# Kernel tuning notes

Measured on AMD Instinct MI355X. Metric: run time of the kernel, lower is better.

The kernel has to match this reference:

```python
import jax, jax.numpy as jnp
import numpy as np

XN = 144
YN = 144
BN_EPS = 1e-5


def setup_inputs() -> dict:
    key = jax.random.key(0)
    k1, k2, k3, k4, k5 = jax.random.split(key, 5)
    B, P, M, F, C = 8, 12000, 32, 9, 64
    pillars = jax.random.normal(k1, (B, P, M, F), dtype=jnp.float32)
    pillar_indices = jax.random.randint(k2, (B, P, 3), 0, 144, dtype=jnp.int64)
    conv_w = jax.random.normal(k3, (C, F), dtype=jnp.float32) * 0.1  # 1x1 conv, no bias
    bn_gamma = jnp.ones((C,), dtype=jnp.float32)
    bn_beta = jnp.zeros((C,), dtype=jnp.float32)
    bn_mean = jax.random.normal(k4, (C,), dtype=jnp.float32) * 0.01
    bn_var = jax.random.uniform(k5, (C,), dtype=jnp.float32, minval=0.5, maxval=1.5)
    return {"pillars": pillars, "pillar_indices": pillar_indices, "conv_w": conv_w,
            "bn_gamma": bn_gamma, "bn_beta": bn_beta, "bn_mean": bn_mean, "bn_var": bn_var}


def reference(pillars, pillar_indices, conv_w, bn_gamma, bn_beta, bn_mean, bn_var):
    # pillars: [B, P, M, F] -> 1x1 conv over feature dim -> [B, C, P, M]
    x = jnp.einsum('bpmf,cf->bcpm', pillars, conv_w)
    # BatchNorm2d (inference) + ReLU
    inv_std = jax.lax.rsqrt(bn_var + BN_EPS)
    x = (x - bn_mean[None, :, None, None]) * (bn_gamma * inv_std)[None, :, None, None] \
        + bn_beta[None, :, None, None]
    x = jax.nn.relu(x)
    # MaxPool2d((1, M)): max over points-per-pillar axis -> [B, C, P]
    feat = jnp.max(x, axis=-1)
    # Scatter pillar features into BEV canvas [C, Xn*Yn]
    y_idx = pillar_indices[:, :, 1]                      # [B, P]
    x_idx = jnp.clip(pillar_indices[:, :, 2], 0, 143)    # [B, P]
    flat_idx = y_idx * XN + x_idx                        # [B, P]

    C = feat.shape[1]

    def scatter_one(f, idx):  # f: [C, P], idx: [P]
        canvas = jnp.zeros((C, XN * YN), dtype=f.dtype)
        return canvas.at[:, idx].set(f)

    out = jax.vmap(scatter_one)(feat, flat_idx)          # [B, C, Xn*Yn]
    return out.reshape(feat.shape[0], C, XN, YN)
```

## Files before the change

### kernel.cpp

```cpp
#include <hip/hip_runtime.h>
#include <hip/hip_bf16.h>
#include <stdint.h>

#define NB 8
#define NP 12000
#define NM 32
#define NF 9
#define NC 64
#define NX 144
#define NCELL (144*144)

#define PPW 8
#define FEAT_WAVES ((NB*NP)/PPW)
#define FEAT_BLOCKS (FEAT_WAVES/4)
#define TILES_PER_B (NCELL/64)

typedef __attribute__((ext_vector_type(8)))  short bfrag8;
typedef __attribute__((ext_vector_type(16))) float accf16;
typedef float f32x4u __attribute__((ext_vector_type(4), aligned(4)));

#define WS_BTAB  0
#define WS_SHIFT 2048
#define WS_WIN   4096
#define WS_CELL  667648
#define WS_NEED  (WS_CELL + (size_t)NB*NCELL*NC*4)

__global__ void winner_prep_kernel(const int* __restrict__ idx, int* __restrict__ winner,
                                   const float* __restrict__ conv_w,
                                   const float* __restrict__ gamma,
                                   const float* __restrict__ beta,
                                   const float* __restrict__ mean,
                                   const float* __restrict__ var,
                                   unsigned short* __restrict__ btab,
                                   float* __restrict__ shift)
{
    int t = blockIdx.x * blockDim.x + threadIdx.x;
    if (t < NB * NP) {
        int b = t / NP;
        int p = t - b * NP;
        int y = idx[t * 3 + 1];
        int x = idx[t * 3 + 2];
        x = x < 0 ? 0 : (x > 143 ? 143 : x);
        y = y < 0 ? 0 : (y > 143 ? 143 : y);
        atomicMax(&winner[b * NCELL + y * NX + x], p);
    }
    if (blockIdx.x == 0) {
        int tt = threadIdx.x;
        if (tt < 128) {
            int ct = tt >> 6, L = tt & 63;
            int c  = ct * 32 + (L & 31);
            int kq = L >> 5;
            float sc = gamma[c] * rsqrtf(var[c] + 1e-5f);
            unsigned short* dst = btab + (ct * 64 + L) * 8;
            #pragma unroll
            for (int j = 0; j < 8; ++j) {
                int k = kq * 8 + j;
                float w = (k < NF) ? conv_w[c * NF + k] * sc : 0.f;
                __hip_bfloat16 h = __float2bfloat16(w);
                dst[j] = *(unsigned short*)&h;
            }
        }
        if (tt < NC) {
            float sc = gamma[tt] * rsqrtf(var[tt] + 1e-5f);
            shift[tt] = beta[tt] - mean[tt] * sc;
        }
    }
}

__device__ __forceinline__ float max16(const accf16& a) {
    float t0 = fmaxf(fmaxf(a[0], a[1]),  fmaxf(a[2], a[3]));
    float t1 = fmaxf(fmaxf(a[4], a[5]),  fmaxf(a[6], a[7]));
    float t2 = fmaxf(fmaxf(a[8], a[9]),  fmaxf(a[10], a[11]));
    float t3 = fmaxf(fmaxf(a[12], a[13]), fmaxf(a[14], a[15]));
    return fmaxf(fmaxf(t0, t1), fmaxf(t2, t3));
}

template <bool COMPACT>
__global__ void __launch_bounds__(256) feat_dense_kernel(
    const float* __restrict__ pillars,
    const unsigned short* __restrict__ btab,
    const float* __restrict__ shift,
    const int*   __restrict__ idx,
    const int*   __restrict__ winner,
    float* __restrict__ feat_cell,
    float* __restrict__ out)
{
    int tid  = threadIdx.x;
    int lane = tid & 63;
    int wave = blockIdx.x * 4 + (tid >> 6);
    int row  = lane & 31;
    int kq   = lane >> 5;
    int b    = wave / (NP / PPW);

    bfrag8 b0 = *(const bfrag8*)(btab + lane * 8);
    bfrag8 b1 = *(const bfrag8*)(btab + (64 + lane) * 8);
    float  sh = shift[lane];
    accf16 z  = {};

    int cellv[PPW];
    bool winv[PPW];
    #pragma unroll
    for (int i = 0; i < PPW; ++i) {
        int pil = wave * PPW + i;
        int y = idx[pil * 3 + 1];
        int x = idx[pil * 3 + 2];
        x = x < 0 ? 0 : (x > 143 ? 143 : x);
        y = y < 0 ? 0 : (y > 143 ? 143 : y);
        int cell = y * NX + x;
        cellv[i] = cell;
        winv[i]  = (winner[b * NCELL + cell] == pil - b * NP);
    }

    const float* wbase = pillars + (size_t)wave * (PPW * NM * NF) + row * NF;

    #pragma unroll
    for (int g = 0; g < PPW / 4; ++g) {
        f32x4u lo[4], hi[4];
        float  e8[4];
        #pragma unroll
        for (int i = 0; i < 4; ++i) {
            const float* base = wbase + (size_t)(g * 4 + i) * (NM * NF);
            lo[i] = *(const f32x4u*)(base);
            hi[i] = *(const f32x4u*)(base + 4);
            e8[i] = base[8];
        }
        #pragma unroll
        for (int i = 0; i < 4; ++i) {
            int pi = g * 4 + i;
            float s[8];
            s[0] = kq ? e8[i] : lo[i][0];
            s[1] = kq ? 0.f   : lo[i][1];
            s[2] = kq ? 0.f   : lo[i][2];
            s[3] = kq ? 0.f   : lo[i][3];
            s[4] = kq ? 0.f   : hi[i][0];
            s[5] = kq ? 0.f   : hi[i][1];
            s[6] = kq ? 0.f   : hi[i][2];
            s[7] = kq ? 0.f   : hi[i][3];
            bfrag8 a;
            #pragma unroll
            for (int j = 0; j < 8; ++j) {
                __hip_bfloat16 h = __float2bfloat16(s[j]);
                a[j] = *(short*)&h;
            }
            accf16 acc0 = __builtin_amdgcn_mfma_f32_32x32x16_bf16(a, b0, z, 0, 0, 0);
            accf16 acc1 = __builtin_amdgcn_mfma_f32_32x32x16_bf16(a, b1, z, 0, 0, 0);

            float v0 = max16(acc0);
            float v1 = max16(acc1);
            v0 = fmaxf(v0, __shfl_xor(v0, 32));
            v1 = fmaxf(v1, __shfl_xor(v1, 32));
            float r = (lane < 32) ? v0 : v1;
            r += sh;
            r = r > 0.f ? r : 0.f;

            if (winv[pi]) {
                if (COMPACT) {
                    feat_cell[((size_t)(b * NCELL + cellv[pi])) * NC + lane] = r;
                } else {
                    out[((size_t)(b * NC + lane)) * NCELL + cellv[pi]] = r;
                }
            }
        }
    }
}

__global__ void __launch_bounds__(256) scatter_t_kernel(
    const int* __restrict__ winner,
    const float* __restrict__ feat_cell,
    float* __restrict__ out)
{
    __shared__ float ld[NC * 68];
    int tile = blockIdx.x;
    int b    = tile / TILES_PER_B;
    int cb   = (tile - b * TILES_PER_B) * 64;
    int t    = threadIdx.x;

    {
        int cell = t >> 2, q = t & 3;
        int w = winner[b * NCELL + cb + cell];
        const f32x4u* src = (const f32x4u*)(feat_cell +
                             ((size_t)(b * NCELL + cb + cell)) * NC);
        #pragma unroll
        for (int k = 0; k < 4; ++k) {
            f32x4u v = {0.f, 0.f, 0.f, 0.f};
            if (w >= 0) v = src[q * 4 + k];
            int c = q * 16 + k * 4;
            ld[(c + 0) * 68 + cell] = v[0];
            ld[(c + 1) * 68 + cell] = v[1];
            ld[(c + 2) * 68 + cell] = v[2];
            ld[(c + 3) * 68 + cell] = v[3];
        }
    }
    __syncthreads();
    {
        int c = t >> 2, qq = t & 3;
        float* o = out + ((size_t)(b * NC + c)) * NCELL + cb + qq * 16;
        const float* lrow = ld + c * 68 + qq * 16;
        #pragma unroll
        for (int k = 0; k < 4; ++k) {
            *(f32x4u*)(o + k * 4) = *(const f32x4u*)(lrow + k * 4);
        }
    }
}

extern "C" void kernel_launch(void* const* d_in, const int* in_sizes, int n_in,
                              void* d_out, int out_size, void* d_ws, size_t ws_size,
                              hipStream_t stream) {
    const float* pillars = (const float*)d_in[0];
    const int*   idx     = (const int*)d_in[1];
    const float* conv_w  = (const float*)d_in[2];
    const float* gamma   = (const float*)d_in[3];
    const float* beta    = (const float*)d_in[4];
    const float* mean    = (const float*)d_in[5];
    const float* var     = (const float*)d_in[6];
    float* out = (float*)d_out;

    char* ws = (char*)d_ws;
    unsigned short* btab      = (unsigned short*)(ws + WS_BTAB);
    float*          shift     = (float*)(ws + WS_SHIFT);
    int*            winner    = (int*)(ws + WS_WIN);
    float*          feat_cell = (float*)(ws + WS_CELL);

    const bool compact = ws_size >= WS_NEED;

    hipMemsetAsync(winner, 0xFF, (size_t)NB * NCELL * sizeof(int), stream);
    winner_prep_kernel<<<(NB * NP + 255) / 256, 256, 0, stream>>>(
        idx, winner, conv_w, gamma, beta, mean, var, btab, shift);

    if (compact) {
        feat_dense_kernel<true><<<FEAT_BLOCKS, 256, 0, stream>>>(
            pillars, btab, shift, idx, winner, feat_cell, out);
        scatter_t_kernel<<<NB * TILES_PER_B, 256, 0, stream>>>(
            winner, feat_cell, out);
    } else {
        hipMemsetAsync(out, 0, (size_t)out_size * sizeof(float), stream);
        feat_dense_kernel<false><<<FEAT_BLOCKS, 256, 0, stream>>>(
            pillars, btab, shift, idx, winner, feat_cell, out);
    }
}
```

Measured before the change: 209.0 us.

## Compact winning pillars into a list and compute features only for winners

A new compaction kernel scans the winner map and appends (cell, pillar) pairs to a list using a global atomic counter. The feature kernel then gathers and computes only those pillars, skipping the reads and MFMA work for pillars overwritten by a later duplicate in the same cell. The scatter kernel's load mapping is also reworked so consecutive threads handle consecutive cells. The trade-offs are an extra launch, a single contended atomic counter, and gathered rather than streaming pillar reads.

After: 241.7 us. 15.6% more time.

```diff
diff --git a/kernel.cpp b/kernel.cpp
--- a/kernel.cpp
+++ b/kernel.cpp
@@ -21,8 +21,10 @@
 
 #define WS_BTAB  0
 #define WS_SHIFT 2048
+#define WS_CNT   2304
 #define WS_WIN   4096
-#define WS_CELL  667648
+#define WS_LIST  667648
+#define WS_CELL  1435648
 #define WS_NEED  (WS_CELL + (size_t)NB*NCELL*NC*4)
 
 __global__ void winner_prep_kernel(const int* __restrict__ idx, int* __restrict__ winner,
@@ -32,7 +34,8 @@
                                    const float* __restrict__ mean,
                                    const float* __restrict__ var,
                                    unsigned short* __restrict__ btab,
-                                   float* __restrict__ shift)
+                                   float* __restrict__ shift,
+                                   int* __restrict__ cnt)
 {
     int t = blockIdx.x * blockDim.x + threadIdx.x;
     if (t < NB * NP) {
@@ -64,6 +67,22 @@
             float sc = gamma[tt] * rsqrtf(var[tt] + 1e-5f);
             shift[tt] = beta[tt] - mean[tt] * sc;
         }
+        if (tt == 200) *cnt = 0;
+    }
+}
+
+__global__ void compact_kernel(const int* __restrict__ winner,
+                               int* __restrict__ cnt,
+                               int2* __restrict__ list)
+{
+    int cell_b = blockIdx.x * blockDim.x + threadIdx.x;
+    if (cell_b < NB * NCELL) {
+        int w = winner[cell_b];
+        if (w >= 0) {
+            int b = cell_b / NCELL;
+            int pos = atomicAdd(cnt, 1);
+            list[pos] = make_int2(cell_b, b * NP + w);
+        }
     }
 }
 
@@ -75,43 +94,36 @@
     return fmaxf(fmaxf(t0, t1), fmaxf(t2, t3));
 }
 
-template <bool COMPACT>
-__global__ void __launch_bounds__(256) feat_dense_kernel(
+__global__ void __launch_bounds__(256) feat_list_kernel(
     const float* __restrict__ pillars,
     const unsigned short* __restrict__ btab,
     const float* __restrict__ shift,
-    const int*   __restrict__ idx,
-    const int*   __restrict__ winner,
-    float* __restrict__ feat_cell,
-    float* __restrict__ out)
+    const int*  __restrict__ cnt,
+    const int2* __restrict__ list,
+    float* __restrict__ feat_cell)
 {
     int tid  = threadIdx.x;
     int lane = tid & 63;
     int wave = blockIdx.x * 4 + (tid >> 6);
-    int row  = lane & 31;
-    int kq   = lane >> 5;
-    int b    = wave / (NP / PPW);
+    int n    = *cnt;
+    int base = wave * PPW;
+    if (base >= n) return;
+
+    int row = lane & 31;
+    int kq  = lane >> 5;
 
     bfrag8 b0 = *(const bfrag8*)(btab + lane * 8);
     bfrag8 b1 = *(const bfrag8*)(btab + (64 + lane) * 8);
     float  sh = shift[lane];
     accf16 z  = {};
 
-    int cellv[PPW];
-    bool winv[PPW];
+    int2 ent[PPW];
     #pragma unroll
     for (int i = 0; i < PPW; ++i) {
-        int pil = wave * PPW + i;
-        int y = idx[pil * 3 + 1];
-        int x = idx[pil * 3 + 2];
-        x = x < 0 ? 0 : (x > 143 ? 143 : x);
-        y = y < 0 ? 0 : (y > 143 ? 143 : y);
-        int cell = y * NX + x;
-        cellv[i] = cell;
-        winv[i]  = (winner[b * NCELL + cell] == pil - b * NP);
-    }
-
-    const float* wbase = pillars + (size_t)wave * (PPW * NM * NF) + row * NF;
+        int j = base + i;
+        j = j < n - 1 ? j : n - 1;
+        ent[i] = list[j];
+    }
 
     #pragma unroll
     for (int g = 0; g < PPW / 4; ++g) {
@@ -119,10 +131,10 @@
         float  e8[4];
         #pragma unroll
         for (int i = 0; i < 4; ++i) {
-            const float* base = wbase + (size_t)(g * 4 + i) * (NM * NF);
-            lo[i] = *(const f32x4u*)(base);
-            hi[i] = *(const f32x4u*)(base + 4);
-            e8[i] = base[8];
+            const float* bp = pillars + (size_t)ent[g * 4 + i].y * (NM * NF) + row * NF;
+            lo[i] = *(const f32x4u*)(bp);
+            hi[i] = *(const f32x4u*)(bp + 4);
+            e8[i] = bp[8];
         }
         #pragma unroll
         for (int i = 0; i < 4; ++i) {
@@ -153,12 +165,89 @@
             r += sh;
             r = r > 0.f ? r : 0.f;
 
+            feat_cell[(size_t)ent[pi].x * NC + lane] = r;
+        }
+    }
+}
+
+__global__ void __launch_bounds__(256) feat_dense_fallback(
+    const float* __restrict__ pillars,
+    const unsigned short* __restrict__ btab,
+    const float* __restrict__ shift,
+    const int*   __restrict__ idx,
+    const int*   __restrict__ winner,
+    float* __restrict__ out)
+{
+    int tid  = threadIdx.x;
+    int lane = tid & 63;
+    int wave = blockIdx.x * 4 + (tid >> 6);
+    int row  = lane & 31;
+    int kq   = lane >> 5;
+    int b    = wave / (NP / PPW);
+
+    bfrag8 b0 = *(const bfrag8*)(btab + lane * 8);
+    bfrag8 b1 = *(const bfrag8*)(btab + (64 + lane) * 8);
+    float  sh = shift[lane];
+    accf16 z  = {};
+
+    int cellv[PPW];
+    bool winv[PPW];
+    #pragma unroll
+    for (int i = 0; i < PPW; ++i) {
+        int pil = wave * PPW + i;
+        int y = idx[pil * 3 + 1];
+        int x = idx[pil * 3 + 2];
+        x = x < 0 ? 0 : (x > 143 ? 143 : x);
+        y = y < 0 ? 0 : (y > 143 ? 143 : y);
+        int cell = y * NX + x;
+        cellv[i] = cell;
+        winv[i]  = (winner[b * NCELL + cell] == pil - b * NP);
+    }
+
+    const float* wbase = pillars + (size_t)wave * (PPW * NM * NF) + row * NF;
+
+    #pragma unroll
+    for (int g = 0; g < PPW / 4; ++g) {
+        f32x4u lo[4], hi[4];
+        float  e8[4];
+        #pragma unroll
+        for (int i = 0; i < 4; ++i) {
+            const float* base = wbase + (size_t)(g * 4 + i) * (NM * NF);
+            lo[i] = *(const f32x4u*)(base);
+            hi[i] = *(const f32x4u*)(base + 4);
+            e8[i] = base[8];
+        }
+        #pragma unroll
+        for (int i = 0; i < 4; ++i) {
+            int pi = g * 4 + i;
+            float s[8];
+            s[0] = kq ? e8[i] : lo[i][0];
+            s[1] = kq ? 0.f   : lo[i][1];
+            s[2] = kq ? 0.f   : lo[i][2];
+            s[3] = kq ? 0.f   : lo[i][3];
+            s[4] = kq ? 0.f   : hi[i][0];
+            s[5] = kq ? 0.f   : hi[i][1];
+            s[6] = kq ? 0.f   : hi[i][2];
+            s[7] = kq ? 0.f   : hi[i][3];
+            bfrag8 a;
+            #pragma unroll
+            for (int j = 0; j < 8; ++j) {
+                __hip_bfloat16 h = __float2bfloat16(s[j]);
+                a[j] = *(short*)&h;
+            }
+            accf16 acc0 = __builtin_amdgcn_mfma_f32_32x32x16_bf16(a, b0, z, 0, 0, 0);
+            accf16 acc1 = __builtin_amdgcn_mfma_f32_32x32x16_bf16(a, b1, z, 0, 0, 0);
+
+            float v0 = max16(acc0);
+            float v1 = max16(acc1);
+            v0 = fmaxf(v0, __shfl_xor(v0, 32));
+            v1 = fmaxf(v1, __shfl_xor(v1, 32));
+            float r = (lane < 32) ? v0 : v1;
+            r += sh;
+            r = r > 0.f ? r : 0.f;
+
             if (winv[pi]) {
-                if (COMPACT) {
-                    feat_cell[((size_t)(b * NCELL + cellv[pi])) * NC + lane] = r;
-                } else {
-                    out[((size_t)(b * NC + lane)) * NCELL + cellv[pi]] = r;
-                }
+                out[((size_t)(b * NC + lane)) * NCELL + cellv[pi]] = r;
             }
         }
     }
@@ -176,15 +265,16 @@
     int t    = threadIdx.x;
 
     {
-        int cell = t >> 2, q = t & 3;
-        int w = winner[b * NCELL + cb + cell];
+        int cell = t & 63;
+        int c0   = (t >> 6) * 16;
+        int win  = winner[b * NCELL + cb + cell];
         const f32x4u* src = (const f32x4u*)(feat_cell +
-                             ((size_t)(b * NCELL + cb + cell)) * NC);
+                             ((size_t)(b * NCELL + cb + cell)) * NC + c0);
         #pragma unroll
         for (int k = 0; k < 4; ++k) {
             f32x4u v = {0.f, 0.f, 0.f, 0.f};
-            if (w >= 0) v = src[q * 4 + k];
-            int c = q * 16 + k * 4;
+            if (win >= 0) v = src[k];
+            int c = c0 + k * 4;
             ld[(c + 0) * 68 + cell] = v[0];
             ld[(c + 1) * 68 + cell] = v[1];
             ld[(c + 2) * 68 + cell] = v[2];
@@ -218,23 +308,27 @@
     char* ws = (char*)d_ws;
     unsigned short* btab      = (unsigned short*)(ws + WS_BTAB);
     float*          shift     = (float*)(ws + WS_SHIFT);
+    int*            cnt       = (int*)(ws + WS_CNT);
     int*            winner    = (int*)(ws + WS_WIN);
+    int2*           list      = (int2*)(ws + WS_LIST);
     float*          feat_cell = (float*)(ws + WS_CELL);
 
     const bool compact = ws_size >= WS_NEED;
 
     hipMemsetAsync(winner, 0xFF, (size_t)NB * NCELL * sizeof(int), stream);
     winner_prep_kernel<<<(NB * NP + 255) / 256, 256, 0, stream>>>(
-        idx, winner, conv_w, gamma, beta, mean, var, btab, shift);
+        idx, winner, conv_w, gamma, beta, mean, var, btab, shift, cnt);
 
     if (compact) {
-        feat_dense_kernel<true><<<FEAT_BLOCKS, 256, 0, stream>>>(
-            pillars, btab, shift, idx, winner, feat_cell, out);
+        compact_kernel<<<(NB * NCELL + 255) / 256, 256, 0, stream>>>(
+            winner, cnt, list);
+        feat_list_kernel<<<FEAT_BLOCKS, 256, 0, stream>>>(
+            pillars, btab, shift, cnt, list, feat_cell);
         scatter_t_kernel<<<NB * TILES_PER_B, 256, 0, stream>>>(
             winner, feat_cell, out);
     } else {
         hipMemsetAsync(out, 0, (size_t)out_size * sizeof(float), stream);
-        feat_dense_kernel<false><<<FEAT_BLOCKS, 256, 0, stream>>>(
-            pillars, btab, shift, idx, winner, feat_cell, out);
-    }
-}
+        feat_dense_fallback<<<FEAT_BLOCKS, 256, 0, stream>>>(
+            pillars, btab, shift, idx, winner, out);
+    }
+}
```
